# Optimization experiments

Hardware: AMD Instinct MI355X
Metric: run time of the kernel (lower is better)

## Reference

```python
import jax, jax.numpy as jnp
import numpy as np

N, E, G, F_IN, D = 50000, 400000, 256, 79, 400
BN_EPS = 1e-5


def setup_inputs() -> dict:
    key = jax.random.key(0)
    ks = jax.random.split(key, 16)
    w = lambda k, s: jax.random.normal(k, s, dtype=jnp.float32) * 0.05
    return {
        "x": jax.random.normal(ks[0], (N, F_IN), dtype=jnp.float32),
        "edge_index": jax.random.randint(ks[1], (2, E), 0, N, dtype=jnp.int32),
        "batch_index": jnp.sort(jax.random.randint(ks[2], (N,), 0, G, dtype=jnp.int32)),
        "num_graphs": G,
        "mlp1_w1": w(ks[3], (F_IN, D)), "mlp1_b1": jnp.zeros(D, jnp.float32),
        "mlp1_bn_g": jnp.ones(D, jnp.float32), "mlp1_bn_b": jnp.zeros(D, jnp.float32),
        "mlp1_bn_m": jnp.zeros(D, jnp.float32), "mlp1_bn_v": jnp.ones(D, jnp.float32),
        "mlp1_w2": w(ks[4], (D, D)), "mlp1_b2": jnp.zeros(D, jnp.float32),
        "mlp2_w1": w(ks[5], (D, D)), "mlp2_b1": jnp.zeros(D, jnp.float32),
        "mlp2_bn_g": jnp.ones(D, jnp.float32), "mlp2_bn_b": jnp.zeros(D, jnp.float32),
        "mlp2_bn_m": jnp.zeros(D, jnp.float32), "mlp2_bn_v": jnp.ones(D, jnp.float32),
        "mlp2_w2": w(ks[6], (D, D)), "mlp2_b2": jnp.zeros(D, jnp.float32),
        "out1_w": w(ks[7], (D, D)), "out1_b": jnp.zeros(D, jnp.float32),
        "out2_w": w(ks[8], (D, D)), "out2_b": jnp.zeros(D, jnp.float32),
        "out3_w": w(ks[9], (D, D)), "out3_b": jnp.zeros(D, jnp.float32),
        "out_w": w(ks[10], (2 * D, 1)), "out_b": jnp.zeros(1, jnp.float32),
        "eps1": jnp.full((1,), 5e-5, jnp.float32),
        "eps2": jnp.full((1,), 5e-5, jnp.float32),
        "eps3": jnp.full((1,), 5e-5, jnp.float32),
    }


def _bn(z, g, b, m, v):
    # BatchNorm1d in inference mode (running stats)
    return (z - m) * jax.lax.rsqrt(v + BN_EPS) * g + b


def _gin(h, src, dst, eps, w1, b1, g, bb, m, v, w2, b2):
    n = h.shape[0]
    agg = jax.ops.segment_sum(h[src], dst, num_segments=n)  # [N, d] scatter-add
    z = (1.0 + eps) * h + agg
    z = jax.nn.relu(_bn(z @ w1 + b1, g, bb, m, v))
    return jax.nn.relu(z @ w2 + b2)


def reference(x, edge_index, batch_index, num_graphs,
              mlp1_w1, mlp1_b1, mlp1_bn_g, mlp1_bn_b, mlp1_bn_m, mlp1_bn_v, mlp1_w2, mlp1_b2,
              mlp2_w1, mlp2_b1, mlp2_bn_g, mlp2_bn_b, mlp2_bn_m, mlp2_bn_v, mlp2_w2, mlp2_b2,
              out1_w, out1_b, out2_w, out2_b, out3_w, out3_b, out_w, out_b,
              eps1, eps2, eps3):
    src, dst = edge_index[0], edge_index[1]
    h = _gin(x, src, dst, eps1[0], mlp1_w1, mlp1_b1, mlp1_bn_g, mlp1_bn_b, mlp1_bn_m, mlp1_bn_v, mlp1_w2, mlp1_b2)
    h = jnp.tanh(h @ out1_w + out1_b)
    h = _gin(h, src, dst, eps2[0], mlp2_w1, mlp2_b1, mlp2_bn_g, mlp2_bn_b, mlp2_bn_m, mlp2_bn_v, mlp2_w2, mlp2_b2)
    h = jnp.tanh(h @ out2_w + out2_b)
    h = _gin(h, src, dst, eps3[0], mlp2_w1, mlp2_b1, mlp2_bn_g, mlp2_bn_b, mlp2_bn_m, mlp2_bn_v, mlp2_w2, mlp2_b2)
    h = jnp.tanh(h @ out3_w + out3_b)
    # dropout is identity in eval mode
    mx = jax.ops.segment_max(h, batch_index, num_segments=num_graphs)   # global_max_pool
    sm = jax.ops.segment_sum(h, batch_index, num_segments=num_graphs)
    cnt = jax.ops.segment_sum(jnp.ones((h.shape[0], 1), h.dtype), batch_index, num_segments=num_graphs)
    mn = sm / jnp.maximum(cnt, 1.0)                                      # global_mean_pool
    pooled = jnp.concatenate([mx, mn], axis=1)                           # [G, 2D]
    return pooled @ out_w + out_b
```

## Files before the change

### kernel.cpp

```cpp
#include <hip/hip_runtime.h>
#include <math.h>

#define NN 50000
#define NE 400000
#define NG 256
#define FIN 79
#define DD 400
#define LDK 416
#define LDK1 96
#define XP 80
#define NPAD 512
#define BN_EPS_F 1e-5f

#define SCAN_B 256
#define SCAN_NB ((NN + SCAN_B - 1) / SCAN_B)

typedef unsigned short u16;
typedef unsigned short ushort8 __attribute__((ext_vector_type(8)));
typedef unsigned short ushort4v __attribute__((ext_vector_type(4)));
typedef short short8 __attribute__((ext_vector_type(8)));
typedef float floatx4 __attribute__((ext_vector_type(4)));

__device__ inline u16 f2bf(float f) {
    unsigned int u = __builtin_bit_cast(unsigned int, f);
    u += 0x7fffu + ((u >> 16) & 1u);
    return (u16)(u >> 16);
}
__device__ inline float bf2f(u16 s) {
    unsigned int u = ((unsigned int)s) << 16;
    return __builtin_bit_cast(float, u);
}
__device__ inline float fast_tanh(float x) {
    float e = __expf(2.0f * x);
    return 1.0f - 2.0f / (e + 1.0f);
}

__device__ __forceinline__ void gld_lds16(const u16* g, u16* l) {
    __builtin_amdgcn_global_load_lds(
        (const __attribute__((address_space(1))) unsigned int*)(size_t)(g),
        (__attribute__((address_space(3))) unsigned int*)(unsigned int)(size_t)(l),
        16, 0, 0);
}

__global__ void k_gstart(const int* __restrict__ batch, int* __restrict__ gstart) {
    int g = blockIdx.x * blockDim.x + threadIdx.x;
    if (g > NG) return;
    int lo = 0, hi = NN;
    while (lo < hi) {
        int mid = (lo + hi) >> 1;
        if (batch[mid] < g) lo = mid + 1; else hi = mid;
    }
    gstart[g] = lo;
}

__global__ void k_zero_int(int* __restrict__ p, int n) {
    int i = blockIdx.x * blockDim.x + threadIdx.x;
    if (i < n) p[i] = 0;
}
__global__ void k_hist(const int* __restrict__ dst, int* __restrict__ deg) {
    int e = blockIdx.x * blockDim.x + threadIdx.x;
    if (e < NE) atomicAdd(&deg[dst[e]], 1);
}

__global__ void k_scan_a(const int* __restrict__ deg, int* __restrict__ bsum) {
    __shared__ int red[SCAN_B];
    int i = blockIdx.x * SCAN_B + threadIdx.x;
    red[threadIdx.x] = (i < NN) ? deg[i] : 0;
    __syncthreads();
    for (int s = SCAN_B / 2; s > 0; s >>= 1) {
        if (threadIdx.x < s) red[threadIdx.x] += red[threadIdx.x + s];
        __syncthreads();
    }
    if (threadIdx.x == 0) bsum[blockIdx.x] = red[0];
}
__global__ void k_scan_b(const int* __restrict__ bsum, int* __restrict__ boff) {
    __shared__ int buf[SCAN_B];
    int t = threadIdx.x;
    int v = (t < SCAN_NB) ? bsum[t] : 0;
    buf[t] = v;
    __syncthreads();
    for (int off = 1; off < SCAN_B; off <<= 1) {
        int add = (t >= off) ? buf[t - off] : 0;
        __syncthreads();
        buf[t] += add;
        __syncthreads();
    }
    if (t < SCAN_NB) boff[t] = buf[t] - v;
}
__global__ void k_scan_c(const int* __restrict__ deg, const int* __restrict__ boff,
                         int* __restrict__ rowptr, int* __restrict__ cursor) {
    __shared__ int buf[SCAN_B];
    int b = blockIdx.x;
    int i = b * SCAN_B + threadIdx.x;
    int v = (i < NN) ? deg[i] : 0;
    buf[threadIdx.x] = v;
    __syncthreads();
    for (int off = 1; off < SCAN_B; off <<= 1) {
        int add = (threadIdx.x >= off) ? buf[threadIdx.x - off] : 0;
        __syncthreads();
        buf[threadIdx.x] += add;
        __syncthreads();
    }
    int excl = boff[b] + buf[threadIdx.x] - v;
    if (i < NN) { rowptr[i] = excl; cursor[i] = excl; }
    if (b == 0 && threadIdx.x == 0) rowptr[NN] = NE;
}

__global__ void k_fill(const int* __restrict__ src, const int* __restrict__ dst,
                       int* __restrict__ cursor, int* __restrict__ eidx) {
    int e = blockIdx.x * blockDim.x + threadIdx.x;
    if (e < NE) {
        int pos = atomicAdd(&cursor[dst[e]], 1);
        eidx[pos] = src[e];
    }
}

__global__ void k_packw(const float* __restrict__ W, int K, u16* __restrict__ Wt, int ldk) {
    int idx = blockIdx.x * 256 + threadIdx.x;
    int total = NPAD * ldk;
    if (idx >= total) return;
    int n = idx / ldk, k = idx - n * ldk;
    float v = (n < DD && k < K) ? W[(size_t)k * DD + n] : 0.0f;
    Wt[idx] = f2bf(v);
}

__global__ __launch_bounds__(256)
void k_packx(const float* __restrict__ x, u16* __restrict__ xb) {
    int idx = blockIdx.x * 256 + threadIdx.x;
    if (idx >= NN * XP) return;
    int n = idx / XP, c = idx - n * XP;
    xb[idx] = (c < FIN) ? f2bf(x[(size_t)n * FIN + c]) : (u16)0;
}

__global__ __launch_bounds__(256)
void k_agg1(const u16* __restrict__ xb, const int* __restrict__ rowptr,
            const int* __restrict__ eidx, const float* __restrict__ eps,
            u16* __restrict__ z0) {
    int wave = threadIdx.x >> 6, lane = threadIdx.x & 63;
    int n = blockIdx.x * 4 + wave;
    if (lane >= 24) return;
    u16* zr = z0 + (size_t)n * LDK1;
    if (lane >= 20) {
        ushort4v zz = {0, 0, 0, 0};
        *(ushort4v*)&zr[XP + (lane - 20) * 4] = zz;
        return;
    }
    float s = 1.0f + eps[0];
    int c4 = lane * 4;
    ushort4v v = *(const ushort4v*)&xb[(size_t)n * XP + c4];
    float a[4];
    #pragma unroll
    for (int t = 0; t < 4; ++t) a[t] = s * bf2f(v[t]);
    int e0 = rowptr[n], e1 = rowptr[n + 1];
    int i = e0;
    for (; i + 2 <= e1; i += 2) {
        int s0 = eidx[i], s1 = eidx[i + 1];
        ushort4v v0 = *(const ushort4v*)&xb[(size_t)s0 * XP + c4];
        ushort4v v1 = *(const ushort4v*)&xb[(size_t)s1 * XP + c4];
        #pragma unroll
        for (int t = 0; t < 4; ++t) a[t] += bf2f(v0[t]) + bf2f(v1[t]);
    }
    if (i < e1) {
        int s0 = eidx[i];
        ushort4v v0 = *(const ushort4v*)&xb[(size_t)s0 * XP + c4];
        #pragma unroll
        for (int t = 0; t < 4; ++t) a[t] += bf2f(v0[t]);
    }
    ushort4v o;
    #pragma unroll
    for (int t = 0; t < 4; ++t) o[t] = f2bf(a[t]);
    *(ushort4v*)&zr[c4] = o;
}

__global__ __launch_bounds__(256)
void k_agg(const u16* __restrict__ h, const int* __restrict__ rowptr,
           const int* __restrict__ eidx, const float* __restrict__ eps,
           u16* __restrict__ z) {
    int wave = threadIdx.x >> 6, lane = threadIdx.x & 63;
    int n = blockIdx.x * 4 + wave;
    if (lane >= 52) return;
    float s = 1.0f + eps[0];
    int c8 = lane * 8;
    ushort8 v = *(const ushort8*)(h + (size_t)n * LDK + c8);
    float a[8];
    #pragma unroll
    for (int t = 0; t < 8; ++t) a[t] = s * bf2f(v[t]);
    int e0 = rowptr[n], e1 = rowptr[n + 1];
    int i = e0;
    for (; i + 2 <= e1; i += 2) {
        int s0 = eidx[i], s1 = eidx[i + 1];
        ushort8 v0 = *(const ushort8*)(h + (size_t)s0 * LDK + c8);
        ushort8 v1 = *(const ushort8*)(h + (size_t)s1 * LDK + c8);
        #pragma unroll
        for (int t = 0; t < 8; ++t) a[t] += bf2f(v0[t]) + bf2f(v1[t]);
    }
    if (i < e1) {
        int s0 = eidx[i];
        ushort8 v0 = *(const ushort8*)(h + (size_t)s0 * LDK + c8);
        #pragma unroll
        for (int t = 0; t < 8; ++t) a[t] += bf2f(v0[t]);
    }
    ushort8 o;
    #pragma unroll
    for (int t = 0; t < 8; ++t) o[t] = f2bf(a[t]);
    *(ushort8*)(z + (size_t)n * LDK + c8) = o;
}

#define CSTR 136
__global__ __launch_bounds__(256, 3)
void k_gemm(const u16* __restrict__ A, int lda, int ktiles,
            const u16* __restrict__ Wt,
            const float* __restrict__ bias,
            const float* __restrict__ bng, const float* __restrict__ bnb,
            const float* __restrict__ bnm, const float* __restrict__ bnv,
            u16* __restrict__ Y, int mode)
{
    __shared__ u16 smem[128 * CSTR];
    u16* As = smem;
    u16* Bs = smem + 128 * 32;
    u16* Cs = smem;

    int tid = threadIdx.x;
    int wave = tid >> 6, lane = tid & 63;
    int wm = wave & 1, wn = wave >> 1;
    int m0 = blockIdx.x * 128;
    int n0 = blockIdx.y * 128;

    int rr = lane >> 2;
    int cc = lane & 3;
    int lm = lane & 15;
    int q  = lane >> 4;

    bool nactive = (n0 + wn * 64) < LDK;

    floatx4 acc[4][4] = {};

    for (int kt = 0; kt < ktiles; ++kt) {
        int k0 = kt * 32;
        #pragma unroll
        for (int j = 0; j < 2; ++j) {
            int row = wave * 32 + j * 16 + rr;
            int sw = (row ^ (row >> 2)) & 3;
            int gr = m0 + row; gr = gr < NN ? gr : NN - 1;
            gld_lds16(A + (size_t)gr * lda + k0 + ((cc ^ sw) << 3),
                      &As[(wave * 32 + j * 16) * 32]);
            gld_lds16(Wt + (size_t)(n0 + row) * lda + k0 + ((cc ^ sw) << 3),
                      &Bs[(wave * 32 + j * 16) * 32]);
        }
        __syncthreads();

        if (nactive) {
            short8 af[4], bf[4];
            #pragma unroll
            for (int i = 0; i < 4; ++i) {
                int r = wm * 64 + i * 16 + lm;
                int sw = (r ^ (r >> 2)) & 3;
                af[i] = *(const short8*)&As[r * 32 + ((q ^ sw) << 3)];
            }
            #pragma unroll
            for (int j = 0; j < 4; ++j) {
                int r = wn * 64 + j * 16 + lm;
                int sw = (r ^ (r >> 2)) & 3;
                bf[j] = *(const short8*)&Bs[r * 32 + ((q ^ sw) << 3)];
            }
            #pragma unroll
            for (int i = 0; i < 4; ++i)
                #pragma unroll
                for (int j = 0; j < 4; ++j)
                    acc[i][j] = __builtin_amdgcn_mfma_f32_16x16x32_bf16(af[i], bf[j], acc[i][j], 0, 0, 0);
        }
        __syncthreads();
    }

    #pragma unroll
    for (int j = 0; j < 4; ++j) {
        int nl = wn * 64 + j * 16 + lm;
        int n  = n0 + nl;
        bool live = n < DD;
        float bias_c = 0.0f, sc = 1.0f, sh = 0.0f;
        if (live) {
            bias_c = bias[n];
            if (mode == 0) {
                sc = bng[n] * rsqrtf(bnv[n] + BN_EPS_F);
                sh = bnb[n] - bnm[n] * sc;
            }
        }
        #pragma unroll
        for (int i = 0; i < 4; ++i) {
            int rl = wm * 64 + i * 16 + q * 4;
            #pragma unroll
            for (int r = 0; r < 4; ++r) {
                u16 o = 0;
                if (live) {
                    float val = acc[i][j][r] + bias_c;
                    if (mode == 0)      val = fmaxf(fmaf(val, sc, sh), 0.0f);
                    else if (mode == 1) val = fmaxf(val, 0.0f);
                    else                val = fast_tanh(val);
                    o = f2bf(val);
                }
                Cs[(rl + r) * CSTR + nl] = o;
            }
        }
    }
    __syncthreads();

    int row = tid >> 1, half = tid & 1;
    int m = m0 + row;
    if (m < NN) {
        #pragma unroll
        for (int k = 0; k < 8; ++k) {
            int coloff = half * 64 + k * 8;
            int n = n0 + coloff;
            if (n < LDK) {
                ushort8 v = *(const ushort8*)&Cs[row * CSTR + coloff];
                *(ushort8*)&Y[(size_t)m * LDK + n] = v;
            }
        }
    }
}

__global__ void k_pool(const u16* __restrict__ t3, const int* __restrict__ gstart,
                       float* __restrict__ pooled) {
    int g = blockIdx.x;
    int c = blockIdx.y * 128 + threadIdx.x;
    if (c >= DD) return;
    int s = gstart[g], e = gstart[g + 1];
    float mx = -INFINITY, sm = 0.0f;
    for (int n = s; n < e; ++n) {
        float v = bf2f(t3[(size_t)n * LDK + c]);
        mx = fmaxf(mx, v);
        sm += v;
    }
    float cnt = (float)(e - s);
    pooled[(size_t)g * 2 * DD + c] = mx;
    pooled[(size_t)g * 2 * DD + DD + c] = sm / fmaxf(cnt, 1.0f);
}

__global__ void k_final(const float* __restrict__ pooled, const float* __restrict__ w,
                        const float* __restrict__ b, float* __restrict__ out) {
    __shared__ float red[256];
    int g = blockIdx.x;
    float p = 0.0f;
    for (int j = threadIdx.x; j < 2 * DD; j += blockDim.x)
        p += pooled[(size_t)g * 2 * DD + j] * w[j];
    red[threadIdx.x] = p;
    __syncthreads();
    for (int s = 128; s > 0; s >>= 1) {
        if (threadIdx.x < s) red[threadIdx.x] += red[threadIdx.x + s];
        __syncthreads();
    }
    if (threadIdx.x == 0) out[g] = red[0] + b[0];
}

extern "C" void kernel_launch(void* const* d_in, const int* in_sizes, int n_in,
                              void* d_out, int out_size, void* d_ws, size_t ws_size,
                              hipStream_t stream) {
    const float* x     = (const float*)d_in[0];
    const int*   ei    = (const int*)d_in[1];
    const int*   batch = (const int*)d_in[2];
    const float* m1w1  = (const float*)d_in[4];
    const float* m1b1  = (const float*)d_in[5];
    const float* m1g   = (const float*)d_in[6];
    const float* m1bb  = (const float*)d_in[7];
    const float* m1m   = (const float*)d_in[8];
    const float* m1v   = (const float*)d_in[9];
    const float* m1w2  = (const float*)d_in[10];
    const float* m1b2  = (const float*)d_in[11];
    const float* m2w1  = (const float*)d_in[12];
    const float* m2b1  = (const float*)d_in[13];
    const float* m2g   = (const float*)d_in[14];
    const float* m2bb  = (const float*)d_in[15];
    const float* m2m   = (const float*)d_in[16];
    const float* m2v   = (const float*)d_in[17];
    const float* m2w2  = (const float*)d_in[18];
    const float* m2b2  = (const float*)d_in[19];
    const float* o1w   = (const float*)d_in[20];
    const float* o1b   = (const float*)d_in[21];
    const float* o2w   = (const float*)d_in[22];
    const float* o2b   = (const float*)d_in[23];
    const float* o3w   = (const float*)d_in[24];
    const float* o3b   = (const float*)d_in[25];
    const float* ow    = (const float*)d_in[26];
    const float* ob    = (const float*)d_in[27];
    const float* eps1  = (const float*)d_in[28];
    const float* eps2  = (const float*)d_in[29];
    const float* eps3  = (const float*)d_in[30];
    const int* srcI = ei;
    const int* dstI = ei + NE;

    u16* buf1 = (u16*)d_ws;
    u16* buf2 = buf1 + (size_t)NN * LDK;
    u16* buf3 = buf2 + (size_t)NN * LDK;
    u16* z0   = buf3 + (size_t)NN * LDK;
    u16* w1t  = z0 + (size_t)NN * LDK1;
    u16* m1w2t = w1t + (size_t)NPAD * LDK1;
    u16* m2w1t = m1w2t + (size_t)NPAD * LDK;
    u16* m2w2t = m2w1t + (size_t)NPAD * LDK;
    u16* o1t   = m2w2t + (size_t)NPAD * LDK;
    u16* o2t   = o1t + (size_t)NPAD * LDK;
    u16* o3t   = o2t + (size_t)NPAD * LDK;
    u16* xb    = o3t + (size_t)NPAD * LDK;
    float* pooled = (float*)(xb + (size_t)NN * XP);
    int* gstart = (int*)(pooled + (size_t)NG * 2 * DD);
    int* rowptr = gstart + (NG + 2);
    int* cursor = rowptr + (NN + 1);
    int* deg    = cursor + NN;
    int* eidx   = deg + NN;
    int* bsum   = eidx + NE;
    int* boff   = bsum + SCAN_NB;

    float* out = (float*)d_out;

    dim3 gemmGrid((NN + 127) / 128, NPAD / 128);

    k_gstart<<<2, 256, 0, stream>>>(batch, gstart);
    k_zero_int<<<(NN + 255) / 256, 256, 0, stream>>>(deg, NN);
    k_hist<<<(NE + 255) / 256, 256, 0, stream>>>(dstI, deg);
    k_scan_a<<<SCAN_NB, SCAN_B, 0, stream>>>(deg, bsum);
    k_scan_b<<<1, SCAN_B, 0, stream>>>(bsum, boff);
    k_scan_c<<<SCAN_NB, SCAN_B, 0, stream>>>(deg, boff, rowptr, cursor);
    k_fill<<<(NE + 255) / 256, 256, 0, stream>>>(srcI, dstI, cursor, eidx);

    int pw1 = (NPAD * LDK1 + 255) / 256;
    int pw = (NPAD * LDK + 255) / 256;
    k_packw<<<pw1, 256, 0, stream>>>(m1w1, FIN, w1t, LDK1);
    k_packw<<<pw, 256, 0, stream>>>(m1w2, DD, m1w2t, LDK);
    k_packw<<<pw, 256, 0, stream>>>(m2w1, DD, m2w1t, LDK);
    k_packw<<<pw, 256, 0, stream>>>(m2w2, DD, m2w2t, LDK);
    k_packw<<<pw, 256, 0, stream>>>(o1w, DD, o1t, LDK);
    k_packw<<<pw, 256, 0, stream>>>(o2w, DD, o2t, LDK);
    k_packw<<<pw, 256, 0, stream>>>(o3w, DD, o3t, LDK);
    k_packx<<<(NN * XP + 255) / 256, 256, 0, stream>>>(x, xb);

    k_agg1<<<NN / 4, 256, 0, stream>>>(xb, rowptr, eidx, eps1, z0);
    k_gemm<<<gemmGrid, 256, 0, stream>>>(z0, LDK1, LDK1 / 32, w1t, m1b1,
                                         m1g, m1bb, m1m, m1v, buf1, 0);
    k_gemm<<<gemmGrid, 256, 0, stream>>>(buf1, LDK, LDK / 32, m1w2t, m1b2,
                                         nullptr, nullptr, nullptr, nullptr, buf2, 1);
    k_gemm<<<gemmGrid, 256, 0, stream>>>(buf2, LDK, LDK / 32, o1t, o1b,
                                         nullptr, nullptr, nullptr, nullptr, buf3, 2);

    k_agg<<<NN / 4, 256, 0, stream>>>(buf3, rowptr, eidx, eps2, buf1);
    k_gemm<<<gemmGrid, 256, 0, stream>>>(buf1, LDK, LDK / 32, m2w1t, m2b1,
                                         m2g, m2bb, m2m, m2v, buf2, 0);
    k_gemm<<<gemmGrid, 256, 0, stream>>>(buf2, LDK, LDK / 32, m2w2t, m2b2,
                                         nullptr, nullptr, nullptr, nullptr, buf1, 1);
    k_gemm<<<gemmGrid, 256, 0, stream>>>(buf1, LDK, LDK / 32, o2t, o2b,
                                         nullptr, nullptr, nullptr, nullptr, buf2, 2);

    k_agg<<<NN / 4, 256, 0, stream>>>(buf2, rowptr, eidx, eps3, buf1);
    k_gemm<<<gemmGrid, 256, 0, stream>>>(buf1, LDK, LDK / 32, m2w1t, m2b1,
                                         m2g, m2bb, m2m, m2v, buf3, 0);
    k_gemm<<<gemmGrid, 256, 0, stream>>>(buf3, LDK, LDK / 32, m2w2t, m2b2,
                                         nullptr, nullptr, nullptr, nullptr, buf1, 1);
    k_gemm<<<gemmGrid, 256, 0, stream>>>(buf1, LDK, LDK / 32, o3t, o3b,
                                         nullptr, nullptr, nullptr, nullptr, buf3, 2);

    k_pool<<<dim3(NG, 4), 128, 0, stream>>>(buf3, gstart, pooled);
    k_final<<<NG, 256, 0, stream>>>(pooled, ow, ob, out);
}
```

Measured before the change: 878.6 us.

## Double GEMM K-tile to 64 with XOR swizzle and grouped block rasterization

Widens the GEMM K tile from 32 to 64, with an 8-chunk XOR swizzle in LDS, so half as many load/sync iterations run per tile. It remaps blocks onto a 1D grid grouped 8 M-tiles by 4 N-tiles for better L2 reuse of A rows across the N tiles. It also raises the occupancy hint from 3 to 4 blocks per CU. Leading dimensions are padded to 448/128 so K is a multiple of 64, which adds some zero-padded MFMA work and extra bytes in the aggregation kernels.

```diff
diff --git a/kernel.cpp b/kernel.cpp
--- a/kernel.cpp
+++ b/kernel.cpp
@@ -6,10 +6,12 @@
 #define NG 256
 #define FIN 79
 #define DD 400
-#define LDK 416
-#define LDK1 96
+#define LDK 448
+#define LDK1 128
 #define XP 80
 #define NPAD 512
+#define BK 64
+#define MT ((NN + 127) / 128)
 #define BN_EPS_F 1e-5f
 
 #define SCAN_B 256
@@ -138,7 +140,7 @@
             u16* __restrict__ z0) {
     int wave = threadIdx.x >> 6, lane = threadIdx.x & 63;
     int n = blockIdx.x * 4 + wave;
-    if (lane >= 24) return;
+    if (lane >= 32) return;
     u16* zr = z0 + (size_t)n * LDK1;
     if (lane >= 20) {
         ushort4v zz = {0, 0, 0, 0};
@@ -178,7 +180,7 @@
            u16* __restrict__ z) {
     int wave = threadIdx.x >> 6, lane = threadIdx.x & 63;
     int n = blockIdx.x * 4 + wave;
-    if (lane >= 52) return;
+    if (lane >= 56) return;
     float s = 1.0f + eps[0];
     int c8 = lane * 8;
     ushort8 v = *(const ushort8*)(h + (size_t)n * LDK + c8);
@@ -207,7 +209,7 @@
 }
 
 #define CSTR 136
-__global__ __launch_bounds__(256, 3)
+__global__ __launch_bounds__(256, 4)
 void k_gemm(const u16* __restrict__ A, int lda, int ktiles,
             const u16* __restrict__ Wt,
             const float* __restrict__ bias,
@@ -217,17 +219,22 @@
 {
     __shared__ u16 smem[128 * CSTR];
     u16* As = smem;
-    u16* Bs = smem + 128 * 32;
+    u16* Bs = smem + 128 * BK;
     u16* Cs = smem;
+
+    int id = blockIdx.x;
+    int mt = (id >> 5) * 8 + (id & 7);
+    int nt = (id & 31) >> 3;
+    if (mt >= MT) return;
+    int m0 = mt * 128;
+    int n0 = nt * 128;
 
     int tid = threadIdx.x;
     int wave = tid >> 6, lane = tid & 63;
     int wm = wave & 1, wn = wave >> 1;
-    int m0 = blockIdx.x * 128;
-    int n0 = blockIdx.y * 128;
-
-    int rr = lane >> 2;
-    int cc = lane & 3;
+
+    int srow = lane >> 3;
+    int sc   = lane & 7;
     int lm = lane & 15;
     int q  = lane >> 4;
 
@@ -236,38 +243,41 @@
     floatx4 acc[4][4] = {};
 
     for (int kt = 0; kt < ktiles; ++kt) {
-        int k0 = kt * 32;
-        #pragma unroll
-        for (int j = 0; j < 2; ++j) {
-            int row = wave * 32 + j * 16 + rr;
-            int sw = (row ^ (row >> 2)) & 3;
+        int k0 = kt * BK;
+        #pragma unroll
+        for (int j = 0; j < 4; ++j) {
+            int row = wave * 32 + j * 8 + srow;
+            int cs = sc ^ (row & 7);
             int gr = m0 + row; gr = gr < NN ? gr : NN - 1;
-            gld_lds16(A + (size_t)gr * lda + k0 + ((cc ^ sw) << 3),
-                      &As[(wave * 32 + j * 16) * 32]);
-            gld_lds16(Wt + (size_t)(n0 + row) * lda + k0 + ((cc ^ sw) << 3),
-                      &Bs[(wave * 32 + j * 16) * 32]);
+            gld_lds16(A + (size_t)gr * lda + k0 + (cs << 3),
+                      &As[(wave * 32 + j * 8) * BK]);
+            gld_lds16(Wt + (size_t)(n0 + row) * lda + k0 + (cs << 3),
+                      &Bs[(wave * 32 + j * 8) * BK]);
         }
         __syncthreads();
 
         if (nactive) {
-            short8 af[4], bf[4];
             #pragma unroll
-            for (int i = 0; i < 4; ++i) {
-                int r = wm * 64 + i * 16 + lm;
-                int sw = (r ^ (r >> 2)) & 3;
-                af[i] = *(const short8*)&As[r * 32 + ((q ^ sw) << 3)];
+            for (int ks = 0; ks < 2; ++ks) {
+                short8 af[4], bf[4];
+                #pragma unroll
+                for (int i = 0; i < 4; ++i) {
+                    int r = wm * 64 + i * 16 + lm;
+                    int ch = (ks * 4 + q) ^ (r & 7);
+                    af[i] = *(const short8*)&As[r * BK + ch * 8];
+                }
+                #pragma unroll
+                for (int j = 0; j < 4; ++j) {
+                    int r = wn * 64 + j * 16 + lm;
+                    int ch = (ks * 4 + q) ^ (r & 7);
+                    bf[j] = *(const short8*)&Bs[r * BK + ch * 8];
+                }
+                #pragma unroll
+                for (int i = 0; i < 4; ++i)
+                    #pragma unroll
+                    for (int j = 0; j < 4; ++j)
+                        acc[i][j] = __builtin_amdgcn_mfma_f32_16x16x32_bf16(af[i], bf[j], acc[i][j], 0, 0, 0);
             }
-            #pragma unroll
-            for (int j = 0; j < 4; ++j) {
-                int r = wn * 64 + j * 16 + lm;
-                int sw = (r ^ (r >> 2)) & 3;
-                bf[j] = *(const short8*)&Bs[r * 32 + ((q ^ sw) << 3)];
-            }
-            #pragma unroll
-            for (int i = 0; i < 4; ++i)
-                #pragma unroll
-                for (int j = 0; j < 4; ++j)
-                    acc[i][j] = __builtin_amdgcn_mfma_f32_16x16x32_bf16(af[i], bf[j], acc[i][j], 0, 0, 0);
         }
         __syncthreads();
     }
@@ -277,12 +287,12 @@
         int nl = wn * 64 + j * 16 + lm;
         int n  = n0 + nl;
         bool live = n < DD;
-        float bias_c = 0.0f, sc = 1.0f, sh = 0.0f;
+        float bias_c = 0.0f, sc2 = 1.0f, sh = 0.0f;
         if (live) {
             bias_c = bias[n];
             if (mode == 0) {
-                sc = bng[n] * rsqrtf(bnv[n] + BN_EPS_F);
-                sh = bnb[n] - bnm[n] * sc;
+                sc2 = bng[n] * rsqrtf(bnv[n] + BN_EPS_F);
+                sh = bnb[n] - bnm[n] * sc2;
             }
         }
         #pragma unroll
@@ -293,7 +303,7 @@
                 u16 o = 0;
                 if (live) {
                     float val = acc[i][j][r] + bias_c;
-                    if (mode == 0)      val = fmaxf(fmaf(val, sc, sh), 0.0f);
+                    if (mode == 0)      val = fmaxf(fmaf(val, sc2, sh), 0.0f);
                     else if (mode == 1) val = fmaxf(val, 0.0f);
                     else                val = fast_tanh(val);
                     o = f2bf(val);
@@ -411,7 +421,7 @@
 
     float* out = (float*)d_out;
 
-    dim3 gemmGrid((NN + 127) / 128, NPAD / 128);
+    int gemmBlocks = ((MT + 7) / 8) * 32;
 
     k_gstart<<<2, 256, 0, stream>>>(batch, gstart);
     k_zero_int<<<(NN + 255) / 256, 256, 0, stream>>>(deg, NN);
@@ -433,28 +443,28 @@
     k_packx<<<(NN * XP + 255) / 256, 256, 0, stream>>>(x, xb);
 
     k_agg1<<<NN / 4, 256, 0, stream>>>(xb, rowptr, eidx, eps1, z0);
-    k_gemm<<<gemmGrid, 256, 0, stream>>>(z0, LDK1, LDK1 / 32, w1t, m1b1,
-                                         m1g, m1bb, m1m, m1v, buf1, 0);
-    k_gemm<<<gemmGrid, 256, 0, stream>>>(buf1, LDK, LDK / 32, m1w2t, m1b2,
-                                         nullptr, nullptr, nullptr, nullptr, buf2, 1);
-    k_gemm<<<gemmGrid, 256, 0, stream>>>(buf2, LDK, LDK / 32, o1t, o1b,
-                                         nullptr, nullptr, nullptr, nullptr, buf3, 2);
+    k_gemm<<<gemmBlocks, 256, 0, stream>>>(z0, LDK1, LDK1 / BK, w1t, m1b1,
+                                           m1g, m1bb, m1m, m1v, buf1, 0);
+    k_gemm<<<gemmBlocks, 256, 0, stream>>>(buf1, LDK, LDK / BK, m1w2t, m1b2,
+                                           nullptr, nullptr, nullptr, nullptr, buf2, 1);
+    k_gemm<<<gemmBlocks, 256, 0, stream>>>(buf2, LDK, LDK / BK, o1t, o1b,
+                                           nullptr, nullptr, nullptr, nullptr, buf3, 2);
 
     k_agg<<<NN / 4, 256, 0, stream>>>(buf3, rowptr, eidx, eps2, buf1);
-    k_gemm<<<gemmGrid, 256, 0, stream>>>(buf1, LDK, LDK / 32, m2w1t, m2b1,
-                                         m2g, m2bb, m2m, m2v, buf2, 0);
-    k_gemm<<<gemmGrid, 256, 0, stream>>>(buf2, LDK, LDK / 32, m2w2t, m2b2,
-                                         nullptr, nullptr, nullptr, nullptr, buf1, 1);
-    k_gemm<<<gemmGrid, 256, 0, stream>>>(buf1, LDK, LDK / 32, o2t, o2b,
-                                         nullptr, nullptr, nullptr, nullptr, buf2, 2);
+    k_gemm<<<gemmBlocks, 256, 0, stream>>>(buf1, LDK, LDK / BK, m2w1t, m2b1,
+                                           m2g, m2bb, m2m, m2v, buf2, 0);
+    k_gemm<<<gemmBlocks, 256, 0, stream>>>(buf2, LDK, LDK / BK, m2w2t, m2b2,
+                                           nullptr, nullptr, nullptr, nullptr, buf1, 1);
+    k_gemm<<<gemmBlocks, 256, 0, stream>>>(buf1, LDK, LDK / BK, o2t, o2b,
+                                           nullptr, nullptr, nullptr, nullptr, buf2, 2);
 
     k_agg<<<NN / 4, 256, 0, stream>>>(buf2, rowptr, eidx, eps3, buf1);
-    k_gemm<<<gemmGrid, 256, 0, stream>>>(buf1, LDK, LDK / 32, m2w1t, m2b1,
-                                         m2g, m2bb, m2m, m2v, buf3, 0);
-    k_gemm<<<gemmGrid, 256, 0, stream>>>(buf3, LDK, LDK / 32, m2w2t, m2b2,
-                                         nullptr, nullptr, nullptr, nullptr, buf1, 1);
-    k_gemm<<<gemmGrid, 256, 0, stream>>>(buf1, LDK, LDK / 32, o3t, o3b,
-                                         nullptr, nullptr, nullptr, nullptr, buf3, 2);
+    k_gemm<<<gemmBlocks, 256, 0, stream>>>(buf1, LDK, LDK / BK, m2w1t, m2b1,
+                                           m2g, m2bb, m2m, m2v, buf3, 0);
+    k_gemm<<<gemmBlocks, 256, 0, stream>>>(buf3, LDK, LDK / BK, m2w2t, m2b2,
+                                           nullptr, nullptr, nullptr, nullptr, buf1, 1);
+    k_gemm<<<gemmBlocks, 256, 0, stream>>>(buf1, LDK, LDK / BK, o3t, o3b,
+                                           nullptr, nullptr, nullptr, nullptr, buf3, 2);
 
     k_pool<<<dim3(NG, 4), 128, 0, stream>>>(buf3, gstart, pooled);
     k_final<<<NG, 256, 0, stream>>>(pooled, ow, ob, out);
```

New measurement: 868.3 us. About the same (-1.2%).
